# Kernel tuning notes

Measured on AMD Instinct MI355X. Metric: run time of the kernel, lower is better.

Reference implementation:

```python
import jax, jax.numpy as jnp
import numpy as np


def setup_inputs() -> dict:
    key = jax.random.key(0)
    ks = jax.random.split(key, 8)
    B, C, H, W = 16, 192, 64, 64
    dt_rank, d_state = 12, 1
    return {
        "x": jax.random.normal(ks[0], (B, C, H, W), dtype=jnp.float32),
        "conv_w": jax.random.normal(ks[1], (C, 1, 5, 5), dtype=jnp.float32) * 0.1,
        "conv_b": jax.random.normal(ks[2], (C,), dtype=jnp.float32) * 0.1,
        "x_proj_w": jax.random.normal(ks[3], (dt_rank + 2 * d_state, C), dtype=jnp.float32) * (C ** -0.5),
        "dt_w": jax.random.normal(ks[4], (C, dt_rank), dtype=jnp.float32) * (dt_rank ** -0.5),
        "dt_b": jax.random.normal(ks[5], (C,), dtype=jnp.float32) * 0.1,
        "A_logs": jnp.zeros((C, d_state), dtype=jnp.float32),  # log(arange(1,d_state+1)) with d_state=1 -> 0
        "Ds": jnp.ones((C,), dtype=jnp.float32),
    }


def reference(x, conv_w, conv_b, x_proj_w, dt_w, dt_b, A_logs, Ds):
    B, C, H, W = x.shape
    L = H * W
    dt_rank = dt_w.shape[1]
    n = A_logs.shape[1]  # d_state
    # depthwise conv2d, kernel 5, padding SAME (=d_conv//2), then SiLU
    x = jax.lax.conv_general_dilated(
        x, conv_w, window_strides=(1, 1), padding='SAME',
        feature_group_count=C, dimension_numbers=('NCHW', 'OIHW', 'NCHW'))
    x = jax.nn.silu(x + conv_b[None, :, None, None])
    xs = x.reshape(B, C, L)  # (b, d, l)
    # x_proj: (dt_rank + 2n, C) @ (b, C, l)
    x_dbl = jnp.einsum('kc,bcl->bkl', x_proj_w, xs)
    dts, Bs, Cs = jnp.split(x_dbl, [dt_rank, dt_rank + n], axis=1)
    # dt projection + softplus (delta_softplus=True with delta_bias)
    delta = jax.nn.softplus(jnp.einsum('cr,brl->bcl', dt_w, dts) + dt_b[None, :, None])  # (b,d,l)
    A = -jnp.exp(A_logs)  # (d, n)
    # selective scan returning the full state trajectory h_t (b,d,n,l):
    # h_t = exp(delta_t * A) * h_{t-1} + delta_t * B_t * u_t
    a = jnp.exp(delta[:, :, None, :] * A[None, :, :, None])        # (b,d,n,l)
    b_el = delta[:, :, None, :] * Bs[:, None, :, :] * xs[:, :, None, :]  # (b,d,n,l)

    def combine(e1, e2):
        a1, b1 = e1
        a2, b2 = e2
        return (a1 * a2, a2 * b1 + b2)

    _, h = jax.lax.associative_scan(combine, (a, b_el), axis=-1)  # h: (b,d,n,l)
    state = h.reshape(B, C * n, L)
    # y = C_t * h_t + D * u (fp32, d_state=1 broadcast)
    y = state.astype(jnp.float32) * Cs.astype(jnp.float32) + xs * Ds[:, None]
    return y.reshape(B, C, H, W)
```

## Files before the change

### kernel.cpp

```cpp
#include <hip/hip_runtime.h>
#include <hip/hip_bf16.h>
#include <cstddef>

#define BB 16
#define CC 192
#define HH 64
#define WW 64
#define LL 4096
#define DTR 12
#define KK 14
#define NSL 8

__device__ __forceinline__ float silu_f(float v) {
  return v / (1.f + __expf(-v));
}

__global__ __launch_bounds__(256) void conv_silu_kernel(
    const float* __restrict__ x, const float* __restrict__ cw,
    const float* __restrict__ cb, float* __restrict__ xs) {
  const int bc = blockIdx.x;
  const int c = bc % CC;
  const int tid = threadIdx.x;
  const int lane = tid & 63;
  const int wv = tid >> 6;
  const int oy0 = wv * 16;

  float w[25];
#pragma unroll
  for (int k = 0; k < 25; ++k) w[k] = cw[c * 25 + k];
  const float bias = cb[c];

  const float* xp = x + (size_t)bc * LL + lane;
  float* op = xs + (size_t)bc * LL + lane;

  float rv[20];
#pragma unroll
  for (int r = 0; r < 20; ++r) {
    const int gr = oy0 + r - 2;
    float v = 0.f;
    if ((unsigned)gr < 64u) v = xp[gr * 64];
    rv[r] = v;
  }

  float acc[5];
#pragma unroll
  for (int i = 0; i < 5; ++i) acc[i] = 0.f;

#pragma unroll
  for (int r = 0; r < 20; ++r) {
    float v = rv[r];
    float vm2 = __shfl_up(v, 2u, 64);
    float vm1 = __shfl_up(v, 1u, 64);
    float vp1 = __shfl_down(v, 1u, 64);
    float vp2 = __shfl_down(v, 2u, 64);
    if (lane < 2) vm2 = 0.f;
    if (lane < 1) vm1 = 0.f;
    if (lane > 62) vp1 = 0.f;
    if (lane > 61) vp2 = 0.f;
    float t[5] = {vm2, vm1, v, vp1, vp2};
#pragma unroll
    for (int ky = 0; ky < 5; ++ky) {
      if (r >= ky && (r - ky) < 16) {
        float s = acc[(r - ky) % 5];
#pragma unroll
        for (int kx = 0; kx < 5; ++kx) s += w[ky * 5 + kx] * t[kx];
        acc[(r - ky) % 5] = s;
      }
    }
    if (r >= 4) {
      const int yf = oy0 + r - 4;
      float a = acc[(r - 4) % 5] + bias;
      op[yf * 64] = silu_f(a);
      acc[(r - 4) % 5] = 0.f;
    }
  }
}

__global__ __launch_bounds__(64) void proj_part_kernel(
    const float* __restrict__ xs, const float* __restrict__ xpw,
    float* __restrict__ part) {
  const int l0 = blockIdx.x * 256;
  const int b = blockIdx.y;
  const int sl = blockIdx.z;
  const int lane = threadIdx.x;
  const int c0 = sl * 24;

  float4 acc[KK];
#pragma unroll
  for (int k = 0; k < KK; ++k) acc[k] = make_float4(0.f, 0.f, 0.f, 0.f);

  const float* bp = xs + ((size_t)(b * CC + c0)) * LL + l0 + lane * 4;
#pragma unroll 6
  for (int cc = 0; cc < 24; ++cc) {
    const float4 v = *(const float4*)(bp + (size_t)cc * LL);
    const int c = c0 + cc;
#pragma unroll
    for (int k = 0; k < KK; ++k) {
      const float w = xpw[k * CC + c];
      acc[k].x += w * v.x;
      acc[k].y += w * v.y;
      acc[k].z += w * v.z;
      acc[k].w += w * v.w;
    }
  }

  float* pp = part + ((size_t)((b * NSL + sl) * KK)) * LL + l0 + lane * 4;
#pragma unroll
  for (int k = 0; k < KK; ++k)
    *(float4*)(pp + (size_t)k * LL) = acc[k];
}

__global__ __launch_bounds__(256) void proj_reduce_kernel(
    const float* __restrict__ part, float* __restrict__ xdbl) {
  const int f = blockIdx.x * 256 + threadIdx.x;
  const int k = blockIdx.y;
  const int b = blockIdx.z;
  const size_t off = (size_t)f * 4;

  float4 s = make_float4(0.f, 0.f, 0.f, 0.f);
#pragma unroll
  for (int sl = 0; sl < NSL; ++sl) {
    const float4 v = *(const float4*)(
        part + ((size_t)((b * NSL + sl) * KK + k)) * LL + off);
    s.x += v.x; s.y += v.y; s.z += v.z; s.w += v.w;
  }
  *(float4*)(xdbl + ((size_t)(b * KK + k)) * LL + off) = s;
}

__global__ __launch_bounds__(512) void scan_kernel(
    const float* __restrict__ xs, const float* __restrict__ xdbl,
    const float* __restrict__ dtw, const float* __restrict__ dtb,
    const float* __restrict__ A_logs, const float* __restrict__ Ds,
    float* __restrict__ y) {
  const int bc = blockIdx.x;
  const int b = bc / CC;
  const int c = bc - b * CC;
  const int tid = threadIdx.x;
  const int lane = tid & 63;
  const int wv = tid >> 6;

  const float Ac = -__expf(A_logs[c]);
  const float Dc = Ds[c];
  float dw[DTR];
#pragma unroll
  for (int r = 0; r < DTR; ++r) dw[r] = dtw[c * DTR + r];
  const float db = dtb[c];

  const float* xp = xs + (size_t)bc * LL;
  const float* xb = xdbl + (size_t)b * KK * LL;
  float* yp = y + (size_t)bc * LL;

  __shared__ float segA[8];
  __shared__ float segB[8];

  float alpha[8], beta[8];
  float aggA[2], aggB[2];

#pragma unroll
  for (int ck = 0; ck < 2; ++ck) {
    const int base = wv * 512 + ck * 256 + lane * 4;
    const float4 x4 = *(const float4*)(xp + base);
    const float4 B4 = *(const float4*)(xb + 12 * LL + base);
    const float4 C4 = *(const float4*)(xb + 13 * LL + base);
    float zx = db, zy = db, zz_ = db, zw = db;
#pragma unroll
    for (int r = 0; r < DTR; ++r) {
      const float4 d4 = *(const float4*)(xb + r * LL + base);
      zx += dw[r] * d4.x;
      zy += dw[r] * d4.y;
      zz_ += dw[r] * d4.z;
      zw += dw[r] * d4.w;
    }
    const float zq[4] = {zx, zy, zz_, zw};
    float Pl = 1.f, hl = 0.f;
#pragma unroll
    for (int q = 0; q < 4; ++q) {
      const float z = zq[q];
      const float delta = (z > 15.f) ? z : __logf(1.f + __expf(z));
      const float a = __expf(delta * Ac);
      const float be = delta * ((&B4.x)[q]) * ((&x4.x)[q]);
      hl = a * hl + be;
      Pl = Pl * a;
      alpha[ck * 4 + q] = Pl * ((&C4.x)[q]);
      beta[ck * 4 + q] = hl * ((&C4.x)[q]) + ((&x4.x)[q]) * Dc;
    }
    aggA[ck] = Pl;
    aggB[ck] = hl;
  }

  float iA[2], iB[2];
#pragma unroll
  for (int ck = 0; ck < 2; ++ck) { iA[ck] = aggA[ck]; iB[ck] = aggB[ck]; }
#pragma unroll
  for (int s = 1; s < 64; s <<= 1) {
    float pA[2], pB[2];
#pragma unroll
    for (int ck = 0; ck < 2; ++ck) {
      pA[ck] = __shfl_up(iA[ck], (unsigned)s, 64);
      pB[ck] = __shfl_up(iB[ck], (unsigned)s, 64);
    }
    if (lane >= s) {
#pragma unroll
      for (int ck = 0; ck < 2; ++ck) {
        iB[ck] = iA[ck] * pB[ck] + iB[ck];
        iA[ck] = iA[ck] * pA[ck];
      }
    }
  }
  float eA[2], eB[2], tA[2], tB[2];
#pragma unroll
  for (int ck = 0; ck < 2; ++ck) {
    eA[ck] = __shfl_up(iA[ck], 1u, 64);
    eB[ck] = __shfl_up(iB[ck], 1u, 64);
    if (lane == 0) { eA[ck] = 1.f; eB[ck] = 0.f; }
    tA[ck] = __shfl(iA[ck], 63, 64);
    tB[ck] = __shfl(iB[ck], 63, 64);
  }

  float Pe[2], he[2];
  float SP = 1.f, Sh = 0.f;
#pragma unroll
  for (int ck = 0; ck < 2; ++ck) {
    Pe[ck] = SP * eA[ck];
    he[ck] = eA[ck] * Sh + eB[ck];
    Sh = tA[ck] * Sh + tB[ck];
    SP = SP * tA[ck];
  }

  if (lane == 0) { segA[wv] = SP; segB[wv] = Sh; }
  __syncthreads();
  float carry = 0.f;
  for (int i = 0; i < wv; ++i) carry = segA[i] * carry + segB[i];

#pragma unroll
  for (int ck = 0; ck < 2; ++ck) {
    const float G = Pe[ck] * carry + he[ck];
    const int base = wv * 512 + ck * 256 + lane * 4;
    float4 o;
    o.x = alpha[ck * 4 + 0] * G + beta[ck * 4 + 0];
    o.y = alpha[ck * 4 + 1] * G + beta[ck * 4 + 1];
    o.z = alpha[ck * 4 + 2] * G + beta[ck * 4 + 2];
    o.w = alpha[ck * 4 + 3] * G + beta[ck * 4 + 3];
    *(float4*)(yp + base) = o;
  }
}

extern "C" void kernel_launch(void* const* d_in, const int* in_sizes, int n_in,
                              void* d_out, int out_size, void* d_ws,
                              size_t ws_size, hipStream_t stream) {
  const float* x        = (const float*)d_in[0];
  const float* conv_w   = (const float*)d_in[1];
  const float* conv_b   = (const float*)d_in[2];
  const float* x_proj_w = (const float*)d_in[3];
  const float* dt_w     = (const float*)d_in[4];
  const float* dt_b     = (const float*)d_in[5];
  const float* A_logs   = (const float*)d_in[6];
  const float* Ds       = (const float*)d_in[7];
  float* out = (float*)d_out;

  char* ws = (char*)d_ws;
  const size_t plane_bytes = (size_t)BB * CC * LL * sizeof(float);
  const size_t xdbl_bytes  = (size_t)BB * KK * LL * sizeof(float);
  float* xs   = (float*)ws;
  float* xdbl = (float*)(ws + plane_bytes);
  float* part = (float*)(ws + plane_bytes + xdbl_bytes);

  conv_silu_kernel<<<dim3(BB * CC), 256, 0, stream>>>(x, conv_w, conv_b, xs);
  proj_part_kernel<<<dim3(LL / 256, BB, NSL), 64, 0, stream>>>(
      xs, x_proj_w, part);
  proj_reduce_kernel<<<dim3(LL / 4 / 256, KK, BB), 256, 0, stream>>>(
      part, xdbl);
  scan_kernel<<<dim3(BB * CC), 512, 0, stream>>>(xs, xdbl, dt_w, dt_b,
                                                 A_logs, Ds, out);
}
```

Measured before the change: 174.9 us.

## Fuse partial-sum reduction with dt projection and materialize delta plane

Replaces the projection reduce kernel with one that sums the split-channel partials, writes B and C rows, and applies the dt projection plus softplus to produce a full per-channel delta plane. The scan kernel then reads precomputed delta, B and C instead of loading 12 dt rows and redoing the projection and softplus per element. The aim is to cut per-block loads and transcendental work in the scan. The cost is a full (B, C, L) delta tensor written to and read back from global memory. The reduce grid is also small and each wave redundantly sums the same 12 dt rows.

```diff
diff --git a/kernel.cpp b/kernel.cpp
--- a/kernel.cpp
+++ b/kernel.cpp
@@ -110,26 +110,74 @@
     *(float4*)(pp + (size_t)k * LL) = acc[k];
 }
 
-__global__ __launch_bounds__(256) void proj_reduce_kernel(
-    const float* __restrict__ part, float* __restrict__ xdbl) {
-  const int f = blockIdx.x * 256 + threadIdx.x;
-  const int k = blockIdx.y;
-  const int b = blockIdx.z;
-  const size_t off = (size_t)f * 4;
-
-  float4 s = make_float4(0.f, 0.f, 0.f, 0.f);
+__global__ __launch_bounds__(512) void reduce_delta_kernel(
+    const float* __restrict__ part, const float* __restrict__ dtw,
+    const float* __restrict__ dtb, float* __restrict__ delta,
+    float* __restrict__ Bsp, float* __restrict__ Csp) {
+  const int b = blockIdx.y;
+  const int l0 = blockIdx.x * 256;
+  const int tid = threadIdx.x;
+  const int lane = tid & 63;
+  const int g = tid >> 6;
+  const size_t l4 = (size_t)l0 + lane * 4;
+
+  const float* pb = part + (size_t)b * NSL * KK * LL + l4;
+
+  float4 dts[DTR];
+#pragma unroll
+  for (int r = 0; r < DTR; ++r) dts[r] = make_float4(0.f, 0.f, 0.f, 0.f);
 #pragma unroll
   for (int sl = 0; sl < NSL; ++sl) {
-    const float4 v = *(const float4*)(
-        part + ((size_t)((b * NSL + sl) * KK + k)) * LL + off);
-    s.x += v.x; s.y += v.y; s.z += v.z; s.w += v.w;
-  }
-  *(float4*)(xdbl + ((size_t)(b * KK + k)) * LL + off) = s;
+    const float* ps = pb + (size_t)sl * KK * LL;
+#pragma unroll
+    for (int r = 0; r < DTR; ++r) {
+      const float4 v = *(const float4*)(ps + (size_t)r * LL);
+      dts[r].x += v.x; dts[r].y += v.y; dts[r].z += v.z; dts[r].w += v.w;
+    }
+  }
+
+  if (g == 0) {
+    float4 sb = make_float4(0.f, 0.f, 0.f, 0.f);
+    float4 sc = make_float4(0.f, 0.f, 0.f, 0.f);
+#pragma unroll
+    for (int sl = 0; sl < NSL; ++sl) {
+      const float* ps = pb + (size_t)sl * KK * LL;
+      const float4 vb = *(const float4*)(ps + (size_t)12 * LL);
+      const float4 vc = *(const float4*)(ps + (size_t)13 * LL);
+      sb.x += vb.x; sb.y += vb.y; sb.z += vb.z; sb.w += vb.w;
+      sc.x += vc.x; sc.y += vc.y; sc.z += vc.z; sc.w += vc.w;
+    }
+    *(float4*)(Bsp + (size_t)b * LL + l4) = sb;
+    *(float4*)(Csp + (size_t)b * LL + l4) = sc;
+  }
+
+  const int c0 = g * 24;
+  float* dp = delta + ((size_t)(b * CC + c0)) * LL + l4;
+#pragma unroll 4
+  for (int cc = 0; cc < 24; ++cc) {
+    const int c = c0 + cc;
+    const float zb = dtb[c];
+    float zx = zb, zy = zb, zz = zb, zw = zb;
+#pragma unroll
+    for (int r = 0; r < DTR; ++r) {
+      const float w = dtw[c * DTR + r];
+      zx += w * dts[r].x;
+      zy += w * dts[r].y;
+      zz += w * dts[r].z;
+      zw += w * dts[r].w;
+    }
+    float4 d;
+    d.x = (zx > 15.f) ? zx : __logf(1.f + __expf(zx));
+    d.y = (zy > 15.f) ? zy : __logf(1.f + __expf(zy));
+    d.z = (zz > 15.f) ? zz : __logf(1.f + __expf(zz));
+    d.w = (zw > 15.f) ? zw : __logf(1.f + __expf(zw));
+    *(float4*)(dp + (size_t)cc * LL) = d;
+  }
 }
 
 __global__ __launch_bounds__(512) void scan_kernel(
-    const float* __restrict__ xs, const float* __restrict__ xdbl,
-    const float* __restrict__ dtw, const float* __restrict__ dtb,
+    const float* __restrict__ xs, const float* __restrict__ delta,
+    const float* __restrict__ Bsp, const float* __restrict__ Csp,
     const float* __restrict__ A_logs, const float* __restrict__ Ds,
     float* __restrict__ y) {
   const int bc = blockIdx.x;
@@ -141,13 +189,11 @@
 
   const float Ac = -__expf(A_logs[c]);
   const float Dc = Ds[c];
-  float dw[DTR];
-#pragma unroll
-  for (int r = 0; r < DTR; ++r) dw[r] = dtw[c * DTR + r];
-  const float db = dtb[c];
 
   const float* xp = xs + (size_t)bc * LL;
-  const float* xb = xdbl + (size_t)b * KK * LL;
+  const float* ddp = delta + (size_t)bc * LL;
+  const float* bpp = Bsp + (size_t)b * LL;
+  const float* cpp = Csp + (size_t)b * LL;
   float* yp = y + (size_t)bc * LL;
 
   __shared__ float segA[8];
@@ -160,25 +206,16 @@
   for (int ck = 0; ck < 2; ++ck) {
     const int base = wv * 512 + ck * 256 + lane * 4;
     const float4 x4 = *(const float4*)(xp + base);
-    const float4 B4 = *(const float4*)(xb + 12 * LL + base);
-    const float4 C4 = *(const float4*)(xb + 13 * LL + base);
-    float zx = db, zy = db, zz_ = db, zw = db;
-#pragma unroll
-    for (int r = 0; r < DTR; ++r) {
-      const float4 d4 = *(const float4*)(xb + r * LL + base);
-      zx += dw[r] * d4.x;
-      zy += dw[r] * d4.y;
-      zz_ += dw[r] * d4.z;
-      zw += dw[r] * d4.w;
-    }
-    const float zq[4] = {zx, zy, zz_, zw};
+    const float4 d4 = *(const float4*)(ddp + base);
+    const float4 B4 = *(const float4*)(bpp + base);
+    const float4 C4 = *(const float4*)(cpp + base);
+
     float Pl = 1.f, hl = 0.f;
 #pragma unroll
     for (int q = 0; q < 4; ++q) {
-      const float z = zq[q];
-      const float delta = (z > 15.f) ? z : __logf(1.f + __expf(z));
-      const float a = __expf(delta * Ac);
-      const float be = delta * ((&B4.x)[q]) * ((&x4.x)[q]);
+      const float dl = (&d4.x)[q];
+      const float a = __expf(dl * Ac);
+      const float be = dl * ((&B4.x)[q]) * ((&x4.x)[q]);
       hl = a * hl + be;
       Pl = Pl * a;
       alpha[ck * 4 + q] = Pl * ((&C4.x)[q]);
@@ -260,16 +297,19 @@
 
   char* ws = (char*)d_ws;
   const size_t plane_bytes = (size_t)BB * CC * LL * sizeof(float);
-  const size_t xdbl_bytes  = (size_t)BB * KK * LL * sizeof(float);
-  float* xs   = (float*)ws;
-  float* xdbl = (float*)(ws + plane_bytes);
-  float* part = (float*)(ws + plane_bytes + xdbl_bytes);
+  const size_t part_bytes  = (size_t)BB * NSL * KK * LL * sizeof(float);
+  const size_t bl_bytes    = (size_t)BB * LL * sizeof(float);
+  float* xs    = (float*)ws;
+  float* part  = (float*)(ws + plane_bytes);
+  float* delta = (float*)(ws + plane_bytes + part_bytes);
+  float* Bsp   = (float*)(ws + 2 * plane_bytes + part_bytes);
+  float* Csp   = (float*)(ws + 2 * plane_bytes + part_bytes + bl_bytes);
 
   conv_silu_kernel<<<dim3(BB * CC), 256, 0, stream>>>(x, conv_w, conv_b, xs);
   proj_part_kernel<<<dim3(LL / 256, BB, NSL), 64, 0, stream>>>(
       xs, x_proj_w, part);
-  proj_reduce_kernel<<<dim3(LL / 4 / 256, KK, BB), 256, 0, stream>>>(
-      part, xdbl);
-  scan_kernel<<<dim3(BB * CC), 512, 0, stream>>>(xs, xdbl, dt_w, dt_b,
+  reduce_delta_kernel<<<dim3(LL / 256, BB), 512, 0, stream>>>(
+      part, dt_w, dt_b, delta, Bsp, Csp);
+  scan_kernel<<<dim3(BB * CC), 512, 0, stream>>>(xs, delta, Bsp, Csp,
                                                  A_logs, Ds, out);
 }
```

After: 208.6 us. 19.3% more time.
